# Optimization experiments

Measured on AMD Instinct MI355X. Metric: run time of the kernel, lower is better.

The kernel has to match this reference:

```python
import jax, jax.numpy as jnp
import numpy as np

DIM = 1024
RANK = 16


def setup_inputs() -> dict:
    key = jax.random.key(0)
    ks = jax.random.split(key, 9)
    s = 0.02
    return {
        "x": jax.random.normal(ks[0], (2, 4096, DIM), dtype=jnp.float32),
        "W_qkv": jax.random.normal(ks[1], (3 * DIM, DIM), dtype=jnp.float32) * s,
        "b_qkv": jax.random.normal(ks[2], (3 * DIM,), dtype=jnp.float32) * s,
        "A_q": jax.random.normal(ks[3], (RANK, DIM), dtype=jnp.float32) * s,
        "B_q": jax.random.normal(ks[4], (DIM, RANK), dtype=jnp.float32) * s,
        "A_k": jax.random.normal(ks[5], (RANK, DIM), dtype=jnp.float32) * s,
        "B_k": jax.random.normal(ks[6], (DIM, RANK), dtype=jnp.float32) * s,
        "A_v": jax.random.normal(ks[7], (RANK, DIM), dtype=jnp.float32) * s,
        "B_v": jax.random.normal(ks[8], (DIM, RANK), dtype=jnp.float32) * s,
        "alpha": jnp.float32(0.5),
    }


def reference(x, W_qkv, b_qkv, A_q, B_q, A_k, B_k, A_v, B_v, alpha):
    # base fused QKV projection: [B, S, 3*dim]
    qkv = jnp.einsum("bsd,od->bso", x, W_qkv) + b_qkv
    # low-rank adapters: x @ A.T @ B.T, rank=16
    lora_q = jnp.einsum("bsr,dr->bsd", jnp.einsum("bsd,rd->bsr", x, A_q), B_q)
    lora_k = jnp.einsum("bsr,dr->bsd", jnp.einsum("bsd,rd->bsr", x, A_k), B_k)
    lora_v = jnp.einsum("bsr,dr->bsd", jnp.einsum("bsd,rd->bsr", x, A_v), B_v)
    # scaled add into q/k/v slices (concat order matches torch slice layout)
    delta = jnp.concatenate([lora_q, lora_k, lora_v], axis=-1)
    return qkv + alpha * delta
```

## Files before the change

kernel.cpp:

```cpp
#include <hip/hip_runtime.h>
#include <stdint.h>

#define DIM    1024
#define RANK   16
#define M_TOT  8192
#define N_TOT  3072
#define K_TOT  1024

#define BM 256
#define BN 256
#define BK 32
#define NT (K_TOT / BK)
#define SLOT_H   16384
#define SLOT_V   2048
#define B_OFF_H  8192
#define B_OFF_V  1024

typedef __attribute__((ext_vector_type(8))) short  s8v;
typedef __attribute__((ext_vector_type(4))) float  f4v;

__device__ __forceinline__ unsigned short f2bf(float f) {
    union { float f; unsigned int u; } v; v.f = f;
    unsigned int u = v.u;
    u += 0x7FFFu + ((u >> 16) & 1u);
    return (unsigned short)(u >> 16);
}

__device__ __forceinline__ void gload_lds16(const unsigned short* g,
                                            unsigned short* l) {
    __builtin_amdgcn_global_load_lds(
        (const __attribute__((address_space(1))) void*)g,
        (__attribute__((address_space(3))) void*)l,
        16, 0, 0);
}

__global__ __launch_bounds__(256)
void prep(const float4* __restrict__ x, ushort4* __restrict__ xb,
          const float* __restrict__ W,
          const float* __restrict__ Aq, const float* __restrict__ Bq,
          const float* __restrict__ Ak, const float* __restrict__ Bk,
          const float* __restrict__ Av, const float* __restrict__ Bv,
          const float* __restrict__ alpha_p,
          unsigned short* __restrict__ Wb) {
    const int tid = threadIdx.x;
    if (blockIdx.x < 2048) {
        int i = blockIdx.x * 256 + tid;
        #pragma unroll
        for (int k = 0; k < 4; ++k) {
            float4 v = x[i];
            ushort4 o;
            o.x = f2bf(v.x); o.y = f2bf(v.y); o.z = f2bf(v.z); o.w = f2bf(v.w);
            xb[i] = o;
            i += 2048 * 256;
        }
    } else {
        const int bid2 = blockIdx.x - 2048;
        const int sel  = bid2 >> 6;
        const int rb   = bid2 & 63;
        const float* Am = (sel == 0) ? Aq : (sel == 1) ? Ak : Av;
        const float* Bm = (sel == 0) ? Bq : (sel == 1) ? Bk : Bv;

        __shared__ float sb[16][RANK];
        {
            const int row = rb * 16 + (tid >> 4);
            sb[tid >> 4][tid & 15] = alpha_p[0] * Bm[row * RANK + (tid & 15)];
        }
        __syncthreads();

        float4 a4[RANK];
        #pragma unroll
        for (int r = 0; r < RANK; ++r)
            a4[r] = ((const float4*)(Am + r * DIM))[tid];

        #pragma unroll
        for (int row = 0; row < 16; ++row) {
            const int o = sel * 1024 + rb * 16 + row;
            float4 w = ((const float4*)(W + (size_t)o * DIM))[tid];
            #pragma unroll
            for (int r = 0; r < RANK; ++r) {
                const float s = sb[row][r];
                w.x += s * a4[r].x; w.y += s * a4[r].y;
                w.z += s * a4[r].z; w.w += s * a4[r].w;
            }
            ushort4 ov;
            ov.x = f2bf(w.x); ov.y = f2bf(w.y); ov.z = f2bf(w.z); ov.w = f2bf(w.w);
            ((ushort4*)(Wb + (size_t)o * DIM))[tid] = ov;
        }
    }
}

__global__ __launch_bounds__(512, 2)
void gemm_bt(const unsigned short* __restrict__ Xb,
             const unsigned short* __restrict__ Wb,
             const float* __restrict__ bias,
             float* __restrict__ out) {
    __shared__ __align__(16) unsigned short S[4 * SLOT_H];

    const int tid  = threadIdx.x;
    const int wave = tid >> 6;
    const int lane = tid & 63;
    const int l15  = lane & 15;
    const int lq   = lane >> 4;
    const int wr   = wave >> 2;
    const int wc   = wave & 3;

    const int bid = blockIdx.x;
    const int xcd = bid & 7;
    const int s   = bid >> 3;
    const int bm  = xcd * 4 + s / 12;
    const int bn  = s % 12;

    const unsigned short* aptr[2];
    const unsigned short* bptr[2];
    int aoff[2], boff[2];
    #pragma unroll
    for (int u = 0; u < 2; ++u) {
        const int c   = wave * 2 + u;
        const int row = c * 16 + l15;
        const int col = lq << 3;
        aptr[u] = Xb + (size_t)(bm * BM + row) * K_TOT + col;
        bptr[u] = Wb + (size_t)(bn * BN + row) * K_TOT + col;
        aoff[u] = c * 512;
        boff[u] = B_OFF_H + c * 512;
    }

    #define STAGE(q)                                                         \
    {                                                                        \
        unsigned short* sl = &S[((q) & 3) * SLOT_H];                         \
        const int kk = (q) * BK;                                             \
        gload_lds16(aptr[0] + kk, sl + aoff[0]);                             \
        gload_lds16(aptr[1] + kk, sl + aoff[1]);                             \
        gload_lds16(bptr[0] + kk, sl + boff[0]);                             \
        gload_lds16(bptr[1] + kk, sl + boff[1]);                             \
    }

    f4v acc[8][4] = {};

    #define COMPUTE(q)                                                       \
    {                                                                        \
        const s8v* P = (const s8v*)S + ((q) & 3) * SLOT_V;                   \
        s8v af[8], bf[4];                                                    \
        _Pragma("unroll")                                                    \
        for (int j = 0; j < 4; ++j)                                          \
            bf[j] = P[B_OFF_V + (wc * 4 + j) * 64 + lane];                   \
        _Pragma("unroll")                                                    \
        for (int i = 0; i < 8; ++i)                                          \
            af[i] = P[(wr * 8 + i) * 64 + lane];                             \
        __builtin_amdgcn_s_setprio(1);                                       \
        _Pragma("unroll")                                                    \
        for (int i = 0; i < 8; ++i)                                          \
            _Pragma("unroll")                                                \
            for (int j = 0; j < 4; ++j)                                      \
                acc[i][j] = __builtin_amdgcn_mfma_f32_16x16x32_bf16(         \
                    af[i], bf[j], acc[i][j], 0, 0, 0);                       \
        __builtin_amdgcn_s_setprio(0);                                       \
    }

    #define QSYNC(n)                                                         \
    {                                                                        \
        __builtin_amdgcn_sched_barrier(0);                                   \
        asm volatile("s_waitcnt vmcnt(" #n ")" ::: "memory");                \
        __builtin_amdgcn_s_barrier();                                        \
        __builtin_amdgcn_sched_barrier(0);                                   \
    }

    STAGE(0); STAGE(1); STAGE(2);
    QSYNC(8);

    #pragma unroll 4
    for (int q = 0; q < NT - 4; ++q) {
        STAGE(q + 3);
        COMPUTE(q);
        QSYNC(8);
    }
    STAGE(NT - 1);
    COMPUTE(NT - 4);
    QSYNC(8);
    COMPUTE(NT - 3);
    QSYNC(4);
    COMPUTE(NT - 2);
    QSYNC(0);
    COMPUTE(NT - 1);
    #undef STAGE
    #undef COMPUTE
    #undef QSYNC

    const int col_base = bn * BN + wc * 64;
    const int row_base = bm * BM + wr * 128 + lq * 4;
    #pragma unroll
    for (int j = 0; j < 4; ++j) {
        const int col = col_base + j * 16 + l15;
        const float bv = bias[col];
        #pragma unroll
        for (int i = 0; i < 8; ++i) {
            const int row = row_base + i * 16;
            #pragma unroll
            for (int r = 0; r < 4; ++r)
                out[(size_t)(row + r) * N_TOT + col] = acc[i][j][r] + bv;
        }
    }
}

extern "C" void kernel_launch(void* const* d_in, const int* in_sizes, int n_in,
                              void* d_out, int out_size, void* d_ws, size_t ws_size,
                              hipStream_t stream) {
    const float* x     = (const float*)d_in[0];
    const float* W     = (const float*)d_in[1];
    const float* b     = (const float*)d_in[2];
    const float* Aq    = (const float*)d_in[3];
    const float* Bq    = (const float*)d_in[4];
    const float* Ak    = (const float*)d_in[5];
    const float* Bk    = (const float*)d_in[6];
    const float* Av    = (const float*)d_in[7];
    const float* Bv    = (const float*)d_in[8];
    const float* alpha = (const float*)d_in[9];
    float* out = (float*)d_out;

    unsigned short* xb = (unsigned short*)d_ws;
    unsigned short* Wb = (unsigned short*)((char*)d_ws + (size_t)M_TOT * K_TOT * 2);

    prep<<<2048 + 192, 256, 0, stream>>>((const float4*)x, (ushort4*)xb,
                                         W, Aq, Bq, Ak, Bk, Av, Bv, alpha, Wb);

    gemm_bt<<<(M_TOT / BM) * (N_TOT / BN), 512, 0, stream>>>(xb, Wb, b, out);
}
```

Baseline: 225.8 us.

## Switch GEMM to double-buffered LDS pipeline with higher occupancy target

Reduces the LDS ring from four stages to two (64KB to 32KB per block) and raises the launch-bounds occupancy hint from 2 to 4 blocks per CU. The main loop now issues the next stage, waits for the current one, computes, and then takes an extra barrier before overwriting the buffer. The aim is more resident blocks to hide latency, at the cost of a shallower prefetch and two barriers per K-step. The tighter register budget could also cause spills for the 32 accumulator vectors.

```diff
diff --git a/kernel.cpp b/kernel.cpp
--- a/kernel.cpp
+++ b/kernel.cpp
@@ -89,12 +89,12 @@
     }
 }
 
-__global__ __launch_bounds__(512, 2)
+__global__ __launch_bounds__(512, 4)
 void gemm_bt(const unsigned short* __restrict__ Xb,
              const unsigned short* __restrict__ Wb,
              const float* __restrict__ bias,
              float* __restrict__ out) {
-    __shared__ __align__(16) unsigned short S[4 * SLOT_H];
+    __shared__ __align__(16) unsigned short S[2 * SLOT_H];
 
     const int tid  = threadIdx.x;
     const int wave = tid >> 6;
@@ -126,7 +126,7 @@
 
     #define STAGE(q)                                                         \
     {                                                                        \
-        unsigned short* sl = &S[((q) & 3) * SLOT_H];                         \
+        unsigned short* sl = &S[((q) & 1) * SLOT_H];                         \
         const int kk = (q) * BK;                                             \
         gload_lds16(aptr[0] + kk, sl + aoff[0]);                             \
         gload_lds16(aptr[1] + kk, sl + aoff[1]);                             \
@@ -138,7 +138,7 @@
 
     #define COMPUTE(q)                                                       \
     {                                                                        \
-        const s8v* P = (const s8v*)S + ((q) & 3) * SLOT_V;                   \
+        const s8v* P = (const s8v*)S + ((q) & 1) * SLOT_V;                   \
         s8v af[8], bf[4];                                                    \
         _Pragma("unroll")                                                    \
         for (int j = 0; j < 4; ++j)                                          \
@@ -156,34 +156,37 @@
         __builtin_amdgcn_s_setprio(0);                                       \
     }
 
-    #define QSYNC(n)                                                         \
+    #define PUBSYNC(n)                                                       \
     {                                                                        \
         __builtin_amdgcn_sched_barrier(0);                                   \
         asm volatile("s_waitcnt vmcnt(" #n ")" ::: "memory");                \
         __builtin_amdgcn_s_barrier();                                        \
         __builtin_amdgcn_sched_barrier(0);                                   \
     }
-
-    STAGE(0); STAGE(1); STAGE(2);
-    QSYNC(8);
-
-    #pragma unroll 4
-    for (int q = 0; q < NT - 4; ++q) {
-        STAGE(q + 3);
+    #define ENDSYNC()                                                        \
+    {                                                                        \
+        __builtin_amdgcn_sched_barrier(0);                                   \
+        __builtin_amdgcn_s_barrier();                                        \
+        __builtin_amdgcn_sched_barrier(0);                                   \
+    }
+
+    STAGE(0);
+
+    #pragma unroll 2
+    for (int q = 0; q < NT; ++q) {
+        if (q + 1 < NT) {
+            STAGE(q + 1);
+            PUBSYNC(4);
+        } else {
+            PUBSYNC(0);
+        }
         COMPUTE(q);
-        QSYNC(8);
-    }
-    STAGE(NT - 1);
-    COMPUTE(NT - 4);
-    QSYNC(8);
-    COMPUTE(NT - 3);
-    QSYNC(4);
-    COMPUTE(NT - 2);
-    QSYNC(0);
-    COMPUTE(NT - 1);
+        if (q + 1 < NT) ENDSYNC();
+    }
     #undef STAGE
     #undef COMPUTE
-    #undef QSYNC
+    #undef PUBSYNC
+    #undef ENDSYNC
 
     const int col_base = bn * BN + wc * 64;
     const int row_base = bm * BM + wr * 128 + lq * 4;
```

Measured after the change: 737.7 us. 227% more time.

## Split GEMM K-step into two half-tiles with interleaved A/B staging

Applied to the files above, without the earlier changes.

Splits each K-step's MFMA work into two halves of four row-fragments each. The A-tile prefetch is issued before the first half and the B-tile prefetch before the second, with extra workgroup barriers around each half to keep waves in lockstep, aiming for finer overlap of global-to-LDS loads with MFMA. It also lowers the launch-bounds occupancy hint from 2 to 1 block per CU, which frees registers but may reduce latency hiding. The added barriers per iteration could cost more than the finer interleaving gains.

```diff
diff --git a/kernel.cpp b/kernel.cpp
--- a/kernel.cpp
+++ b/kernel.cpp
@@ -13,7 +13,6 @@
 #define NT (K_TOT / BK)
 #define SLOT_H   16384
 #define SLOT_V   2048
-#define B_OFF_H  8192
 #define B_OFF_V  1024
 
 typedef __attribute__((ext_vector_type(8))) short  s8v;
@@ -89,7 +88,7 @@
     }
 }
 
-__global__ __launch_bounds__(512, 2)
+__global__ __launch_bounds__(512, 1)
 void gemm_bt(const unsigned short* __restrict__ Xb,
              const unsigned short* __restrict__ Wb,
              const float* __restrict__ bias,
@@ -121,69 +120,91 @@
         aptr[u] = Xb + (size_t)(bm * BM + row) * K_TOT + col;
         bptr[u] = Wb + (size_t)(bn * BN + row) * K_TOT + col;
         aoff[u] = c * 512;
-        boff[u] = B_OFF_H + c * 512;
-    }
-
-    #define STAGE(q)                                                         \
+        boff[u] = 8192 + c * 512;
+    }
+
+    #define STAGE_A(q)                                                       \
     {                                                                        \
         unsigned short* sl = &S[((q) & 3) * SLOT_H];                         \
         const int kk = (q) * BK;                                             \
         gload_lds16(aptr[0] + kk, sl + aoff[0]);                             \
         gload_lds16(aptr[1] + kk, sl + aoff[1]);                             \
+    }
+    #define STAGE_B(q)                                                       \
+    {                                                                        \
+        unsigned short* sl = &S[((q) & 3) * SLOT_H];                         \
+        const int kk = (q) * BK;                                             \
         gload_lds16(bptr[0] + kk, sl + boff[0]);                             \
         gload_lds16(bptr[1] + kk, sl + boff[1]);                             \
     }
 
     f4v acc[8][4] = {};
 
-    #define COMPUTE(q)                                                       \
+    #define TILE(q, DOST, WN, LAST)                                          \
     {                                                                        \
-        const s8v* P = (const s8v*)S + ((q) & 3) * SLOT_V;                   \
-        s8v af[8], bf[4];                                                    \
-        _Pragma("unroll")                                                    \
-        for (int j = 0; j < 4; ++j)                                          \
-            bf[j] = P[B_OFF_V + (wc * 4 + j) * 64 + lane];                   \
-        _Pragma("unroll")                                                    \
-        for (int i = 0; i < 8; ++i)                                          \
-            af[i] = P[(wr * 8 + i) * 64 + lane];                             \
+        const s8v* PA = (const s8v*)S + ((q) & 3) * SLOT_V;                  \
+        const s8v* PB = PA + B_OFF_V;                                        \
+        s8v af[4], bf[4];                                                    \
+                                                      \
+        _Pragma("unroll")                                                    \
+        for (int j = 0; j < 4; ++j) bf[j] = PB[(wc * 4 + j) * 64 + lane];    \
+        _Pragma("unroll")                                                    \
+        for (int i = 0; i < 4; ++i) af[i] = PA[(wr * 8 + i) * 64 + lane];    \
+        if (DOST) STAGE_A((q) + 3);                                          \
+        __builtin_amdgcn_s_barrier();                                        \
+        asm volatile("s_waitcnt lgkmcnt(0)" ::: "memory");                   \
+        __builtin_amdgcn_sched_barrier(0);                                   \
         __builtin_amdgcn_s_setprio(1);                                       \
         _Pragma("unroll")                                                    \
-        for (int i = 0; i < 8; ++i)                                          \
+        for (int i = 0; i < 4; ++i)                                          \
             _Pragma("unroll")                                                \
             for (int j = 0; j < 4; ++j)                                      \
                 acc[i][j] = __builtin_amdgcn_mfma_f32_16x16x32_bf16(         \
                     af[i], bf[j], acc[i][j], 0, 0, 0);                       \
         __builtin_amdgcn_s_setprio(0);                                       \
-    }
-
-    #define QSYNC(n)                                                         \
-    {                                                                        \
+        __builtin_amdgcn_s_barrier();                                        \
+                                                      \
+        _Pragma("unroll")                                                    \
+        for (int i = 0; i < 4; ++i) af[i] = PA[(wr * 8 + 4 + i) * 64 + lane];\
+        if (DOST) STAGE_B((q) + 3);                                          \
+        __builtin_amdgcn_s_barrier();                                        \
+        asm volatile("s_waitcnt lgkmcnt(0)" ::: "memory");                   \
         __builtin_amdgcn_sched_barrier(0);                                   \
-        asm volatile("s_waitcnt vmcnt(" #n ")" ::: "memory");                \
-        __builtin_amdgcn_s_barrier();                                        \
-        __builtin_amdgcn_sched_barrier(0);                                   \
-    }
-
-    STAGE(0); STAGE(1); STAGE(2);
-    QSYNC(8);
+        __builtin_amdgcn_s_setprio(1);                                       \
+        _Pragma("unroll")                                                    \
+        for (int i = 0; i < 4; ++i)                                          \
+            _Pragma("unroll")                                                \
+            for (int j = 0; j < 4; ++j)                                      \
+                acc[4 + i][j] = __builtin_amdgcn_mfma_f32_16x16x32_bf16(     \
+                    af[i], bf[j], acc[4 + i][j], 0, 0, 0);                   \
+        __builtin_amdgcn_s_setprio(0);                                       \
+        if (!(LAST)) {                                                       \
+            __builtin_amdgcn_sched_barrier(0);                               \
+            asm volatile("s_waitcnt vmcnt(" #WN ")" ::: "memory");           \
+            __builtin_amdgcn_s_barrier();                                    \
+            __builtin_amdgcn_sched_barrier(0);                               \
+        }                                                                    \
+    }
+
+    STAGE_A(0); STAGE_B(0);
+    STAGE_A(1); STAGE_B(1);
+    STAGE_A(2); STAGE_B(2);
+    asm volatile("s_waitcnt vmcnt(8)" ::: "memory");
+    __builtin_amdgcn_sched_barrier(0);
+    __builtin_amdgcn_s_barrier();
+    __builtin_amdgcn_sched_barrier(0);
 
     #pragma unroll 4
     for (int q = 0; q < NT - 4; ++q) {
-        STAGE(q + 3);
-        COMPUTE(q);
-        QSYNC(8);
-    }
-    STAGE(NT - 1);
-    COMPUTE(NT - 4);
-    QSYNC(8);
-    COMPUTE(NT - 3);
-    QSYNC(4);
-    COMPUTE(NT - 2);
-    QSYNC(0);
-    COMPUTE(NT - 1);
-    #undef STAGE
-    #undef COMPUTE
-    #undef QSYNC
+        TILE(q, true, 8, false);
+    }
+    TILE(NT - 4, true,  8, false);
+    TILE(NT - 3, false, 4, false);
+    TILE(NT - 2, false, 0, false);
+    TILE(NT - 1, false, 0, true);
+    #undef TILE
+    #undef STAGE_A
+    #undef STAGE_B
 
     const int col_base = bn * BN + wc * 64;
     const int row_base = bm * BM + wr * 128 + lq * 4;
```

Measured after the change: 226.8 us. No clear change (+0.4%).
